# Performance work log

Hardware: AMD Instinct MI355X
Metric: run time of the kernel (lower is better)

Reference implementation:

```python
import jax, jax.numpy as jnp
import numpy as np

D_MODEL = 1024
N_HEADS = 16
HEAD_DIM = D_MODEL // N_HEADS
D_FF = 4 * D_MODEL
LN_EPS = 1e-5


def setup_inputs() -> dict:
    key = jax.random.key(0)
    ks = jax.random.split(key, 12)
    B, T = 16, 512
    s = lambda fan_in: 1.0 / np.sqrt(fan_in)
    inp = {
        'x': jax.random.normal(ks[0], (B, T, D_MODEL), jnp.float32),
        # torch Linear layout: [out_features, in_features]
        'w_qkv': jax.random.normal(ks[1], (3 * D_MODEL, D_MODEL), jnp.float32) * s(D_MODEL),
        'w_proj': jax.random.normal(ks[2], (D_MODEL, D_MODEL), jnp.float32) * s(D_MODEL),
        'w_ff1': jax.random.normal(ks[3], (D_FF, D_MODEL), jnp.float32) * s(D_MODEL),
        'b_ff1': jax.random.normal(ks[4], (D_FF,), jnp.float32) * 0.02,
        'w_ff2': jax.random.normal(ks[5], (D_MODEL, D_FF), jnp.float32) * s(D_FF),
        'b_ff2': jax.random.normal(ks[6], (D_MODEL,), jnp.float32) * 0.02,
        'ln1_g': jnp.ones((D_MODEL,), jnp.float32),
        'ln1_b': jnp.zeros((D_MODEL,), jnp.float32),
        'ln2_g': jnp.ones((D_MODEL,), jnp.float32),
        'ln2_b': jnp.zeros((D_MODEL,), jnp.float32),
    }
    return inp


def _layernorm(x, g, b):
    mu = jnp.mean(x, axis=-1, keepdims=True)
    var = jnp.var(x, axis=-1, keepdims=True)
    return (x - mu) * jax.lax.rsqrt(var + LN_EPS) * g + b


def _block(x, w_qkv, w_proj, w_ff1, b_ff1, w_ff2, b_ff2, ln1_g, ln1_b, ln2_g, ln2_b):
    B, T, _ = x.shape
    a = _layernorm(x, ln1_g, ln1_b)
    qkv = a @ w_qkv.T  # [B,T,3D]
    q, k, v = jnp.split(qkv, 3, axis=-1)
    # [B,H,T,hd]
    rs = lambda t: t.reshape(B, T, N_HEADS, HEAD_DIM).transpose(0, 2, 1, 3)
    q, k, v = rs(q), rs(k), rs(v)
    scale = HEAD_DIM ** -0.5
    att = jnp.einsum('bhqd,bhkd->bhqk', q, k) * scale
    causal = jnp.tril(jnp.ones((T, T), bool))
    att = jnp.where(causal, att, jnp.float32(-10000.0))
    att = jax.nn.softmax(att, axis=-1)
    out = jnp.einsum('bhqk,bhkd->bhqd', att, v)
    out = out.transpose(0, 2, 1, 3).reshape(B, T, D_MODEL)
    x = x + out @ w_proj.T
    f = _layernorm(x, ln2_g, ln2_b)
    f = jax.nn.gelu(f @ w_ff1.T + b_ff1, approximate=False) @ w_ff2.T + b_ff2
    return x + f


def reference(x, w_qkv, w_proj, w_ff1, b_ff1, w_ff2, b_ff2, ln1_g, ln1_b, ln2_g, ln2_b):
    return _block(x, w_qkv, w_proj, w_ff1, b_ff1, w_ff2, b_ff2, ln1_g, ln1_b, ln2_g, ln2_b)
```

## Files before the change

### kernel.cpp

```cpp
#include <hip/hip_runtime.h>
#include <stdint.h>

typedef __bf16 bf16x8_t __attribute__((ext_vector_type(8)));
typedef float f32x4_t __attribute__((ext_vector_type(4)));
typedef unsigned short ushort8_t __attribute__((ext_vector_type(8)));

#define DEV __device__ __forceinline__

DEV unsigned short f2bf(float f) {
  union { float f; uint32_t u; } v; v.f = f;
  uint32_t r = v.u + 0x7FFFu + ((v.u >> 16) & 1u);
  return (unsigned short)(r >> 16);
}

DEV void gl_lds16(const void* g, void* l) {
  __builtin_amdgcn_global_load_lds(
      (const __attribute__((address_space(1))) void*)g,
      (__attribute__((address_space(3))) void*)l, 16, 0, 0);
}

DEV float gelu_f(float x) {
  const float y = x * 0.7071067811865475f;
  const float ay = fabsf(y);
  const float t = __builtin_amdgcn_rcpf(1.0f + 0.3275911f * ay);
  float p = fmaf(t, 1.061405429f, -1.453152027f);
  p = fmaf(t, p, 1.421413741f);
  p = fmaf(t, p, -0.284496736f);
  p = fmaf(t, p, 0.254829592f);
  p *= t;
  const float e = __expf(-ay * ay);
  float erfv = 1.0f - p * e;
  erfv = copysignf(erfv, y);
  return 0.5f * x * (1.0f + erfv);
}

__global__ __launch_bounds__(256) void cvt_all(const float* __restrict__ w0, unsigned short* __restrict__ o0,
                                               const float* __restrict__ w1, unsigned short* __restrict__ o1,
                                               const float* __restrict__ w2, unsigned short* __restrict__ o2,
                                               const float* __restrict__ w3, unsigned short* __restrict__ o3) {
  int i = blockIdx.x * 256 + threadIdx.x;
  const float* in; unsigned short* outp;
  if (i < 786432) { in = w0; outp = o0; }
  else if (i < 1048576) { in = w1; outp = o1; i -= 786432; }
  else if (i < 2097152) { in = w2; outp = o2; i -= 1048576; }
  else { in = w3; outp = o3; i -= 2097152; }
  float4 v = ((const float4*)in)[i];
  ushort4 o;
  o.x = f2bf(v.x); o.y = f2bf(v.y); o.z = f2bf(v.z); o.w = f2bf(v.w);
  ((ushort4*)outp)[i] = o;
}

__global__ __launch_bounds__(256) void ln_kernel(const float* __restrict__ x,
                                                 const float* __restrict__ g,
                                                 const float* __restrict__ b,
                                                 unsigned short* __restrict__ outp) {
  const int row = blockIdx.x * 4 + (threadIdx.x >> 6);
  const int lane = threadIdx.x & 63;
  const float4* xr = (const float4*)(x + (size_t)row * 1024);
  float4 v[4];
  float s = 0.f, s2 = 0.f;
#pragma unroll
  for (int j = 0; j < 4; ++j) {
    v[j] = xr[j * 64 + lane];
    s += v[j].x + v[j].y + v[j].z + v[j].w;
    s2 += v[j].x * v[j].x + v[j].y * v[j].y + v[j].z * v[j].z + v[j].w * v[j].w;
  }
#pragma unroll
  for (int off = 1; off < 64; off <<= 1) {
    s += __shfl_xor(s, off, 64);
    s2 += __shfl_xor(s2, off, 64);
  }
  const float mu = s * (1.0f / 1024.0f);
  const float var = s2 * (1.0f / 1024.0f) - mu * mu;
  const float rstd = rsqrtf(var + 1e-5f);
  ushort4* orow = (ushort4*)(outp + (size_t)row * 1024);
  const float4* gp = (const float4*)g;
  const float4* bp = (const float4*)b;
#pragma unroll
  for (int j = 0; j < 4; ++j) {
    float4 gv = gp[j * 64 + lane], bv = bp[j * 64 + lane];
    ushort4 o;
    o.x = f2bf((v[j].x - mu) * rstd * gv.x + bv.x);
    o.y = f2bf((v[j].y - mu) * rstd * gv.y + bv.y);
    o.z = f2bf((v[j].z - mu) * rstd * gv.z + bv.z);
    o.w = f2bf((v[j].w - mu) * rstd * gv.w + bv.w);
    orow[j * 64 + lane] = o;
  }
}

template <int MODE, int BM>
__global__ __launch_bounds__(256) void gemm_bt(const unsigned short* __restrict__ A,
                                               const unsigned short* __restrict__ B,
                                               float* __restrict__ Cf,
                                               unsigned short* __restrict__ Cb,
                                               const float* __restrict__ bias,
                                               const float* __restrict__ res,
                                               unsigned short* __restrict__ Vt,
                                               int M, int N, int K) {
  constexpr int MI = BM / 32;
  constexpr int RT = 8192 / BM;
  constexpr int ABUF = BM * 32;
  __shared__ unsigned short sA[2][ABUF];
  __shared__ unsigned short sB[2][128 * 32];
  const int tid = threadIdx.x;
  const int w = tid >> 6, lane = tid & 63;
  const int kg = lane >> 4, l16 = lane & 15;
  const int wm = (w & 1) * (BM / 2), wn = (w >> 1) * 64;

  const int cid = blockIdx.y * gridDim.x + blockIdx.x;
  const int colBase = (cid / RT) * 128;
  const int rowBase = (cid % RT) * BM;

  const int sr = (BM == 128) ? (tid >> 2) : ((tid >> 2) & 63);
  const int gc = ((tid & 3) ^ ((sr >> 1) & 3)) * 8;
  const unsigned short* gA = A + (size_t)(rowBase + sr) * K + gc;
  const unsigned short* gB = B + (size_t)(colBase + sr) * K + gc;

  f32x4_t acc[MI][4];
#pragma unroll
  for (int mi = 0; mi < MI; ++mi)
#pragma unroll
    for (int ni = 0; ni < 4; ++ni) acc[mi][ni] = (f32x4_t)0.0f;

  int offA[MI], offB[4];
  const int pc = (kg ^ ((l16 >> 1) & 3)) * 8;
#pragma unroll
  for (int i = 0; i < MI; ++i) offA[i] = (wm + i * 16 + l16) * 32 + pc;
#pragma unroll
  for (int i = 0; i < 4; ++i) offB[i] = (wn + i * 16 + l16) * 32 + pc;

  gl_lds16(gA, &sA[0][tid * 8]);
  if (BM == 128) gl_lds16(gA + (size_t)64 * K, &sA[0][2048 + tid * 8]);
  gl_lds16(gB, &sB[0][tid * 8]);
  gl_lds16(gB + (size_t)64 * K, &sB[0][2048 + tid * 8]);
  gA += 32; gB += 32;

  const int nk = K >> 5;
  for (int kt = 0; kt < nk; ++kt) {
    __syncthreads();
    if (kt + 1 < nk) {
      const int nb = (kt + 1) & 1;
      gl_lds16(gA, &sA[nb][tid * 8]);
      if (BM == 128) gl_lds16(gA + (size_t)64 * K, &sA[nb][2048 + tid * 8]);
      gl_lds16(gB, &sB[nb][tid * 8]);
      gl_lds16(gB + (size_t)64 * K, &sB[nb][2048 + tid * 8]);
      gA += 32; gB += 32;
    }
    const int par = kt & 1;
    bf16x8_t a[MI], b[4];
#pragma unroll
    for (int i = 0; i < MI; ++i) a[i] = *(const bf16x8_t*)(&sA[par][0] + offA[i]);
#pragma unroll
    for (int i = 0; i < 4; ++i) b[i] = *(const bf16x8_t*)(&sB[par][0] + offB[i]);
#pragma unroll
    for (int mi = 0; mi < MI; ++mi)
#pragma unroll
      for (int ni = 0; ni < 4; ++ni)
        acc[mi][ni] = __builtin_amdgcn_mfma_f32_16x16x32_bf16(a[mi], b[ni], acc[mi][ni], 0, 0, 0);
  }

#pragma unroll
  for (int mi = 0; mi < MI; ++mi) {
#pragma unroll
    for (int ni = 0; ni < 4; ++ni) {
      const int col = colBase + wn + ni * 16 + l16;
      if (MODE == 0 && colBase >= 2048) {
        const int c2 = col - 2048;
        const int hh = c2 >> 6, dd = c2 & 63;
        const int rw = rowBase + wm + mi * 16 + kg * 4;
        ushort4 pk;
        pk.x = f2bf(acc[mi][ni][0]);
        pk.y = f2bf(acc[mi][ni][1]);
        pk.z = f2bf(acc[mi][ni][2]);
        pk.w = f2bf(acc[mi][ni][3]);
        *(ushort4*)(Vt + (((size_t)(rw >> 9) * 16 + hh) * 64 + dd) * 512 + (rw & 511)) = pk;
        continue;
      }
      float bv = 0.f;
      if (MODE == 2 || MODE == 3) bv = bias[col];
#pragma unroll
      for (int r = 0; r < 4; ++r) {
        const int row = rowBase + wm + mi * 16 + kg * 4 + r;
        const size_t idx = (size_t)row * N + col;
        float v = acc[mi][ni][r];
        if (MODE == 0) {
          Cb[idx] = f2bf(v);
        } else if (MODE == 1) {
          Cf[idx] = v + res[idx];
        } else if (MODE == 2) {
          Cb[idx] = f2bf(gelu_f(v + bv));
        } else {
          Cf[idx] = v + bv + res[idx];
        }
      }
    }
  }
}

__global__ __launch_bounds__(256) void attn_kernel(const unsigned short* __restrict__ qkv,
                                                   const unsigned short* __restrict__ Vt,
                                                   unsigned short* __restrict__ outp) {
  constexpr int D3 = 3072;
  __shared__ unsigned short sQ[128 * 64];
  __shared__ unsigned short sK[64 * 64];
  __shared__ unsigned short sVt[64 * 64];
  __shared__ unsigned short sP[128 * 72];
  const int tid = threadIdx.x;
  const int w = tid >> 6, lane = tid & 63;
  const int kg = lane >> 4, l16 = lane & 15;
  const int qi = blockIdx.x, h = blockIdx.y, bb = blockIdx.z;
  const int t0 = qi * 128;
  const size_t base = (size_t)bb * 512 * D3 + h * 64;

  const int sr = tid >> 3;
  const int sc = ((tid & 7) ^ (sr & 7)) * 8;

  {
    const unsigned short* g = qkv + base + (size_t)(t0 + sr) * D3 + sc;
    unsigned short* l = sQ + tid * 8;
#pragma unroll
    for (int i = 0; i < 4; ++i) gl_lds16(g + (size_t)32 * i * D3, l + 2048 * i);
  }

  const unsigned short* gVbase = Vt + ((size_t)(bb * 16 + h) * 64 + sr) * 512 + sc;

  bf16x8_t ones;
#pragma unroll
  for (int j = 0; j < 8; ++j) ones[j] = (__bf16)1.0f;

  const int wm = w * 32;
  f32x4_t o[2][4];
  f32x4_t lsum[2];
#pragma unroll
  for (int mi = 0; mi < 2; ++mi) {
    lsum[mi] = (f32x4_t)0.0f;
#pragma unroll
    for (int di = 0; di < 4; ++di) o[mi][di] = (f32x4_t)0.0f;
  }

  const int nkt = (qi + 1) * 2;
  for (int kt = 0; kt < nkt; ++kt) {
    const int k0 = kt * 64;
    __syncthreads();
    {
      const unsigned short* g = qkv + base + 1024 + (size_t)(k0 + sr) * D3 + sc;
      unsigned short* l = sK + tid * 8;
      gl_lds16(g, l);
      gl_lds16(g + (size_t)32 * D3, l + 2048);
    }
    {
      const unsigned short* g = gVbase + k0;
      unsigned short* l = sVt + tid * 8;
      gl_lds16(g, l);
      gl_lds16(g + (size_t)32 * 512, l + 2048);
    }
    __syncthreads();

    const bool active = (k0 <= t0 + wm + 31);
    if (active) {
      f32x4_t s[2][4];
#pragma unroll
      for (int mi = 0; mi < 2; ++mi)
#pragma unroll
        for (int ni = 0; ni < 4; ++ni) s[mi][ni] = (f32x4_t)0.0f;
#pragma unroll
      for (int kd = 0; kd < 2; ++kd) {
        bf16x8_t aq[2], bk[4];
#pragma unroll
        for (int mi = 0; mi < 2; ++mi) {
          const int rr = wm + mi * 16 + l16;
          aq[mi] = *(const bf16x8_t*)(sQ + rr * 64 + (((kd * 4 + kg) ^ (l16 & 7)) * 8));
        }
#pragma unroll
        for (int ni = 0; ni < 4; ++ni) {
          const int rr = ni * 16 + l16;
          bk[ni] = *(const bf16x8_t*)(sK + rr * 64 + (((kd * 4 + kg) ^ (l16 & 7)) * 8));
        }
#pragma unroll
        for (int mi = 0; mi < 2; ++mi)
#pragma unroll
          for (int ni = 0; ni < 4; ++ni)
            s[mi][ni] = __builtin_amdgcn_mfma_f32_16x16x32_bf16(aq[mi], bk[ni], s[mi][ni], 0, 0, 0);
      }
#pragma unroll
      for (int mi = 0; mi < 2; ++mi) {
#pragma unroll
        for (int r = 0; r < 4; ++r) {
          const int q = t0 + wm + mi * 16 + kg * 4 + r;
          const int prow = wm + mi * 16 + kg * 4 + r;
#pragma unroll
          for (int ni = 0; ni < 4; ++ni) {
            const int kk = k0 + ni * 16 + l16;
            const float p = (kk <= q) ? __expf(s[mi][ni][r] * 0.125f) : 0.0f;
            sP[prow * 72 + ni * 16 + l16] = f2bf(p);
          }
        }
      }
#pragma unroll
      for (int kd = 0; kd < 2; ++kd) {
        bf16x8_t ap[2], bv[4];
#pragma unroll
        for (int mi = 0; mi < 2; ++mi)
          ap[mi] = *(const bf16x8_t*)(sP + (wm + mi * 16 + l16) * 72 + kd * 32 + kg * 8);
#pragma unroll
        for (int di = 0; di < 4; ++di) {
          const int dd = di * 16 + l16;
          bv[di] = *(const bf16x8_t*)(sVt + dd * 64 + (((kd * 4 + kg) ^ (l16 & 7)) * 8));
        }
#pragma unroll
        for (int mi = 0; mi < 2; ++mi) {
#pragma unroll
          for (int di = 0; di < 4; ++di)
            o[mi][di] = __builtin_amdgcn_mfma_f32_16x16x32_bf16(ap[mi], bv[di], o[mi][di], 0, 0, 0);
          lsum[mi] = __builtin_amdgcn_mfma_f32_16x16x32_bf16(ap[mi], ones, lsum[mi], 0, 0, 0);
        }
      }
    }
  }

#pragma unroll
  for (int mi = 0; mi < 2; ++mi) {
#pragma unroll
    for (int r = 0; r < 4; ++r) {
      const float inv = 1.0f / lsum[mi][r];
      const int row = t0 + wm + mi * 16 + kg * 4 + r;
      const size_t ob = ((size_t)bb * 512 + row) * 1024 + h * 64;
#pragma unroll
      for (int di = 0; di < 4; ++di)
        outp[ob + di * 16 + l16] = f2bf(o[mi][di][r] * inv);
    }
  }
}

extern "C" void kernel_launch(void* const* d_in, const int* in_sizes, int n_in,
                              void* d_out, int out_size, void* d_ws, size_t ws_size,
                              hipStream_t stream) {
  const float* x      = (const float*)d_in[0];
  const float* w_qkv  = (const float*)d_in[1];
  const float* w_proj = (const float*)d_in[2];
  const float* w_ff1  = (const float*)d_in[3];
  const float* b_ff1  = (const float*)d_in[4];
  const float* w_ff2  = (const float*)d_in[5];
  const float* b_ff2  = (const float*)d_in[6];
  const float* ln1_g  = (const float*)d_in[7];
  const float* ln1_b  = (const float*)d_in[8];
  const float* ln2_g  = (const float*)d_in[9];
  const float* ln2_b  = (const float*)d_in[10];
  float* out = (float*)d_out;
  char* ws = (char*)d_ws;

  unsigned short* wqkv_b  = (unsigned short*)(ws + 0);
  unsigned short* wproj_b = (unsigned short*)(ws + 6291456);
  unsigned short* wff1_b  = (unsigned short*)(ws + 8388608);
  unsigned short* wff2_b  = (unsigned short*)(ws + 16777216);
  unsigned short* a_b     = (unsigned short*)(ws + 25165824);
  float*          x2_f    = (float*)(ws + 41943040);
  unsigned short* vt_b    = (unsigned short*)(ws + 41943040);
  unsigned short* qkv_b   = (unsigned short*)(ws + 75497472);
  unsigned short* attn_b  = (unsigned short*)(ws + 125829120);
  unsigned short* h_b     = qkv_b;

  cvt_all<<<12288, 256, 0, stream>>>(w_qkv, wqkv_b, w_proj, wproj_b, w_ff1, wff1_b, w_ff2, wff2_b);

  ln_kernel<<<2048, 256, 0, stream>>>(x, ln1_g, ln1_b, a_b);
  gemm_bt<0, 128><<<dim3(24, 64), 256, 0, stream>>>(a_b, wqkv_b, nullptr, qkv_b, nullptr, nullptr, vt_b, 8192, 3072, 1024);
  attn_kernel<<<dim3(4, 16, 16), 256, 0, stream>>>(qkv_b, vt_b, attn_b);
  gemm_bt<1, 64><<<dim3(8, 128), 256, 0, stream>>>(attn_b, wproj_b, x2_f, nullptr, nullptr, x, nullptr, 8192, 1024, 1024);
  ln_kernel<<<2048, 256, 0, stream>>>(x2_f, ln2_g, ln2_b, a_b);
  gemm_bt<2, 128><<<dim3(32, 64), 256, 0, stream>>>(a_b, wff1_b, nullptr, h_b, b_ff1, nullptr, nullptr, 8192, 4096, 1024);
  gemm_bt<3, 64><<<dim3(8, 128), 256, 0, stream>>>(h_b, wff2_b, out, nullptr, b_ff2, x2_f, nullptr, 8192, 1024, 4096);
}
```

Measured before the change: 475.9 us.

## Add 256x256 tile FF1 GEMM with 32x32 MFMA and retile proj/FF2

Adds a dedicated FF1 GEMM kernel that gives each block a 256x256 output tile. Each of the 4 waves computes 128x128 with 32x32x16 bf16 MFMA instructions. Operands are double-buffered in LDS through direct global-to-LDS loads, and bias plus GELU are fused into the epilogue. It also switches the proj and FF2 GEMMs from 64-row to 128-row tiles. The goal is more operand reuse per LDS load and less global traffic per FLOP. The cost is higher register pressure (launch_bounds 1), fewer blocks, and uncoalesced bf16 stores in the FF1 epilogue.

```diff
diff --git a/kernel.cpp b/kernel.cpp
--- a/kernel.cpp
+++ b/kernel.cpp
@@ -3,6 +3,7 @@
 
 typedef __bf16 bf16x8_t __attribute__((ext_vector_type(8)));
 typedef float f32x4_t __attribute__((ext_vector_type(4)));
+typedef float f32x16_t __attribute__((ext_vector_type(16)));
 typedef unsigned short ushort8_t __attribute__((ext_vector_type(8)));
 
 #define DEV __device__ __forceinline__
@@ -197,6 +198,95 @@
   }
 }
 
+__global__ __launch_bounds__(256, 1) void gemm_fat_ff1(const unsigned short* __restrict__ A,
+                                                       const unsigned short* __restrict__ B,
+                                                       unsigned short* __restrict__ Cb,
+                                                       const float* __restrict__ bias,
+                                                       int M, int N, int K) {
+  constexpr int BUF = 256 * 32;
+  __shared__ unsigned short sA[2][BUF];
+  __shared__ unsigned short sB[2][BUF];
+  const int tid = threadIdx.x;
+  const int w = tid >> 6, lane = tid & 63;
+  const int l31 = lane & 31, lh = lane >> 5;
+
+  const int cid = blockIdx.y * gridDim.x + blockIdx.x;
+  const int colBase = (cid >> 5) * 256;
+  const int rowBase = (cid & 31) * 256;
+
+  const int sr = tid >> 2;
+  const int gc = ((tid & 3) ^ ((sr >> 1) & 3)) * 8;
+  const unsigned short* gA = A + (size_t)(rowBase + sr) * K + gc;
+  const unsigned short* gB = B + (size_t)(colBase + sr) * K + gc;
+
+  f32x16_t acc[4][4];
+#pragma unroll
+  for (int mi = 0; mi < 4; ++mi)
+#pragma unroll
+    for (int ni = 0; ni < 4; ++ni) acc[mi][ni] = (f32x16_t)0.0f;
+
+  int offA[2][4], offB[2][4];
+#pragma unroll
+  for (int kc = 0; kc < 2; ++kc) {
+    const int pcc = ((kc * 2 + lh) ^ ((l31 >> 1) & 3)) * 8;
+#pragma unroll
+    for (int i = 0; i < 4; ++i) {
+      offA[kc][i] = ((w & 1) * 128 + i * 32 + l31) * 32 + pcc;
+      offB[kc][i] = ((w >> 1) * 128 + i * 32 + l31) * 32 + pcc;
+    }
+  }
+
+#pragma unroll
+  for (int i = 0; i < 4; ++i) {
+    gl_lds16(gA + (size_t)(64 * i) * K, &sA[0][2048 * i + tid * 8]);
+    gl_lds16(gB + (size_t)(64 * i) * K, &sB[0][2048 * i + tid * 8]);
+  }
+  gA += 32; gB += 32;
+
+  const int nk = K >> 5;
+  for (int kt = 0; kt < nk; ++kt) {
+    __syncthreads();
+    if (kt + 1 < nk) {
+      const int nb = (kt + 1) & 1;
+#pragma unroll
+      for (int i = 0; i < 4; ++i) {
+        gl_lds16(gA + (size_t)(64 * i) * K, &sA[nb][2048 * i + tid * 8]);
+        gl_lds16(gB + (size_t)(64 * i) * K, &sB[nb][2048 * i + tid * 8]);
+      }
+      gA += 32; gB += 32;
+    }
+    const int par = kt & 1;
+#pragma unroll
+    for (int kc = 0; kc < 2; ++kc) {
+      bf16x8_t a[4], b[4];
+#pragma unroll
+      for (int i = 0; i < 4; ++i) a[i] = *(const bf16x8_t*)(&sA[par][0] + offA[kc][i]);
+#pragma unroll
+      for (int i = 0; i < 4; ++i) b[i] = *(const bf16x8_t*)(&sB[par][0] + offB[kc][i]);
+#pragma unroll
+      for (int mi = 0; mi < 4; ++mi)
+#pragma unroll
+        for (int ni = 0; ni < 4; ++ni)
+          acc[mi][ni] = __builtin_amdgcn_mfma_f32_32x32x16_bf16(a[mi], b[ni], acc[mi][ni], 0, 0, 0);
+    }
+  }
+
+#pragma unroll
+  for (int mi = 0; mi < 4; ++mi) {
+#pragma unroll
+    for (int ni = 0; ni < 4; ++ni) {
+      const int col = colBase + (w >> 1) * 128 + ni * 32 + l31;
+      const float bv = bias[col];
+      const int rbase = rowBase + (w & 1) * 128 + mi * 32 + 4 * lh;
+#pragma unroll
+      for (int reg = 0; reg < 16; ++reg) {
+        const int row = rbase + (reg & 3) + 8 * (reg >> 2);
+        Cb[(size_t)row * N + col] = f2bf(gelu_f(acc[mi][ni][reg] + bv));
+      }
+    }
+  }
+}
+
 __global__ __launch_bounds__(256) void attn_kernel(const unsigned short* __restrict__ qkv,
                                                    const unsigned short* __restrict__ Vt,
                                                    unsigned short* __restrict__ outp) {
@@ -365,8 +455,8 @@
   ln_kernel<<<2048, 256, 0, stream>>>(x, ln1_g, ln1_b, a_b);
   gemm_bt<0, 128><<<dim3(24, 64), 256, 0, stream>>>(a_b, wqkv_b, nullptr, qkv_b, nullptr, nullptr, vt_b, 8192, 3072, 1024);
   attn_kernel<<<dim3(4, 16, 16), 256, 0, stream>>>(qkv_b, vt_b, attn_b);
-  gemm_bt<1, 64><<<dim3(8, 128), 256, 0, stream>>>(attn_b, wproj_b, x2_f, nullptr, nullptr, x, nullptr, 8192, 1024, 1024);
+  gemm_bt<1, 128><<<dim3(8, 64), 256, 0, stream>>>(attn_b, wproj_b, x2_f, nullptr, nullptr, x, nullptr, 8192, 1024, 1024);
   ln_kernel<<<2048, 256, 0, stream>>>(x2_f, ln2_g, ln2_b, a_b);
-  gemm_bt<2, 128><<<dim3(32, 64), 256, 0, stream>>>(a_b, wff1_b, nullptr, h_b, b_ff1, nullptr, nullptr, 8192, 4096, 1024);
-  gemm_bt<3, 64><<<dim3(8, 128), 256, 0, stream>>>(h_b, wff2_b, out, nullptr, b_ff2, x2_f, nullptr, 8192, 1024, 4096);
-}
+  gemm_fat_ff1<<<dim3(16, 32), 256, 0, stream>>>(a_b, wff1_b, h_b, b_ff1, 8192, 4096, 1024);
+  gemm_bt<3, 128><<<dim3(8, 64), 256, 0, stream>>>(h_b, wff2_b, out, nullptr, b_ff2, x2_f, nullptr, 8192, 1024, 4096);
+}
```

Measured after the change: 486.9 us. 1.02x slower.
